# Kernel tuning notes

Measured on AMD Instinct MI355X. Metric: run time of the kernel, lower is better.

Reference implementation:

```python
import jax, jax.numpy as jnp
import numpy as np

N_NODES = 100000
N_EDGES = 3200000
IN_FEAT = 512
HIDDEN = 256
N_CLASS = 40


def setup_inputs() -> dict:
    key = jax.random.key(0)
    ks = jax.random.split(key, 6)
    x = jax.random.normal(ks[0], (N_NODES, IN_FEAT), dtype=jnp.float32)
    w1 = jax.random.uniform(ks[1], (IN_FEAT, HIDDEN), dtype=jnp.float32)
    b1 = jnp.zeros((HIDDEN,), dtype=jnp.float32)
    w2 = jax.random.uniform(ks[2], (HIDDEN, N_CLASS), dtype=jnp.float32)
    b2 = jnp.zeros((N_CLASS,), dtype=jnp.float32)
    edge_val = jax.random.uniform(ks[3], (N_EDGES,), dtype=jnp.float32)
    edge_row = jax.random.randint(ks[4], (N_EDGES,), 0, N_NODES, dtype=jnp.int32)
    edge_col = jax.random.randint(ks[5], (N_EDGES,), 0, N_NODES, dtype=jnp.int32)
    return {"x": x, "w1": w1, "b1": b1, "w2": w2, "b2": b2,
            "edge_val": edge_val, "edge_row": edge_row, "edge_col": edge_col}


def _graph_conv(h, w, b, edge_val, edge_row, edge_col, n_nodes):
    # dense transform: [N, d_in] @ [d_in, d_out]
    support = h @ w
    # sparse adj @ support via gather + segment_sum (COO SpMM)
    msgs = edge_val[:, None] * support[edge_col]          # [E, d_out]
    agg = jax.ops.segment_sum(msgs, edge_row, num_segments=n_nodes)
    return agg + b


def reference(x, w1, b1, w2, b2, edge_val, edge_row, edge_col):
    n = x.shape[0]
    h = jax.nn.relu(_graph_conv(x, w1, b1, edge_val, edge_row, edge_col, n))
    # dropout is identity in eval mode (training=False)
    out = _graph_conv(h, w2, b2, edge_val, edge_row, edge_col, n)
    return jax.nn.log_softmax(out, axis=1)
```

## Files before the change

kernel.cpp:

```cpp
#include <hip/hip_runtime.h>
#include <cstdint>
#include <cstddef>

#define N_NODES 100000
#define N_EDGES 3200000
#define IN_FEAT 512
#define HIDDEN  256
#define N_CLASS 40
#define S2_STRIDE 48

#define N_BUCKETS 196
#define SC_CHUNK 4096
#define N_SC_BLOCKS 782

#define OFF_SUPPORT1 ((size_t)0)
#define OFF_H        ((size_t)51200000)
#define OFF_SUPPORT2 ((size_t)102400000)
#define OFF_W1T      ((size_t)112000000)
#define OFF_W2T      ((size_t)112262144)
#define OFF_RPTR     ((size_t)112286976)
#define OFF_BCNT     ((size_t)112687104)
#define OFF_BBASE    ((size_t)112688128)
#define OFF_BCUR     ((size_t)112689152)
#define OFF_BINNED   ((size_t)112690176)
#define OFF_SEDGE    ((size_t)138290176)

typedef __attribute__((ext_vector_type(8))) short short8x;
typedef __attribute__((ext_vector_type(4))) float f32x4;
typedef __attribute__((ext_vector_type(8))) unsigned short u16x8;
typedef __attribute__((ext_vector_type(3))) unsigned int u32x3;
typedef __attribute__((ext_vector_type(4))) unsigned int u32x4;

static __device__ __forceinline__ unsigned short f2bf(float f) {
  unsigned u = __float_as_uint(f);
  unsigned r = (u + 0x7FFFu + ((u >> 16) & 1u)) >> 16;
  return (unsigned short)r;
}
static __device__ __forceinline__ float bf2f(unsigned short s) {
  return __uint_as_float(((unsigned)s) << 16);
}
static __device__ __forceinline__ float bflo(unsigned u) {
  return __uint_as_float(u << 16);
}
static __device__ __forceinline__ float bfhi(unsigned u) {
  return __uint_as_float(u & 0xFFFF0000u);
}

static __device__ __forceinline__ void gl16(const void* g, void* l) {
  __builtin_amdgcn_global_load_lds(
      (const __attribute__((address_space(1))) unsigned int*)g,
      (__attribute__((address_space(3))) unsigned int*)l, 16, 0, 0);
}

__global__ __launch_bounds__(256) void k_bincnt(const int* __restrict__ erow,
                                                int* __restrict__ bcnt,
                                                const float* __restrict__ W1,
                                                unsigned short* __restrict__ W1t,
                                                const float* __restrict__ W2,
                                                unsigned short* __restrict__ W2t) {
  int tid = blockIdx.x * 256 + threadIdx.x;
  {
    int n = tid & 255;
    int k = tid >> 8;
    W1t[(size_t)n * IN_FEAT + k] = f2bf(W1[(size_t)k * HIDDEN + n]);
  }
  if (tid < 48 * HIDDEN) {
    int n = tid >> 8;
    int k = tid & 255;
    W2t[n * HIDDEN + k] = (n < N_CLASS) ? f2bf(W2[(size_t)k * N_CLASS + n]) : 0;
  }
  __shared__ int lh[256];
  lh[threadIdx.x] = 0;
  __syncthreads();
  int i = tid;
  int stride = gridDim.x * blockDim.x;
  for (; i < N_EDGES; i += stride) atomicAdd(&lh[erow[i] >> 9], 1);
  __syncthreads();
  if (threadIdx.x < N_BUCKETS) atomicAdd(&bcnt[threadIdx.x], lh[threadIdx.x]);
}

__global__ __launch_bounds__(256) void k_binscan(const int* __restrict__ bcnt,
                                                 int* __restrict__ bbase,
                                                 int* __restrict__ bcur,
                                                 int* __restrict__ rptr) {
  __shared__ int s[256];
  int t = threadIdx.x;
  int v = (t < N_BUCKETS) ? bcnt[t] : 0;
  s[t] = v;
  __syncthreads();
  for (int off = 1; off < 256; off <<= 1) {
    int y = (t >= off) ? s[t - off] : 0;
    __syncthreads();
    s[t] += y;
    __syncthreads();
  }
  if (t < N_BUCKETS) {
    int e = s[t] - v;
    bbase[t] = e;
    bcur[t] = e;
  }
  if (t == 0) {
    bbase[N_BUCKETS] = N_EDGES;
    rptr[N_NODES] = N_EDGES;
  }
}

__global__ __launch_bounds__(256) void k_binscatter(const int* __restrict__ erow,
                                                    const int* __restrict__ ecol,
                                                    const float* __restrict__ eval,
                                                    int* __restrict__ bcur,
                                                    int2* __restrict__ binned) {
  __shared__ int lcnt[256];
  __shared__ int lcur[256];
  const int t = threadIdx.x;
  const int base = blockIdx.x * SC_CHUNK;
  lcnt[t] = 0;
  __syncthreads();
  int rows[16], cols[16], vals[16];
#pragma unroll
  for (int e = 0; e < 16; e++) {
    int i = base + t + e * 256;
    if (i < N_EDGES) {
      rows[e] = erow[i];
      cols[e] = ecol[i];
      vals[e] = __float_as_int(eval[i]);
      atomicAdd(&lcnt[rows[e] >> 9], 1);
    } else {
      rows[e] = -1;
    }
  }
  __syncthreads();
  if (t < N_BUCKETS) lcur[t] = atomicAdd(&bcur[t], lcnt[t]);
  __syncthreads();
#pragma unroll
  for (int e = 0; e < 16; e++) {
    if (rows[e] >= 0) {
      int bkt = rows[e] >> 9;
      int p = atomicAdd(&lcur[bkt], 1);
      binned[p] = make_int2(((rows[e] & 511) << 17) | cols[e], vals[e]);
    }
  }
}

__global__ __launch_bounds__(256) void k_bucket_csr(const int2* __restrict__ binned,
                                                    const int* __restrict__ bbase,
                                                    int* __restrict__ rptr,
                                                    int2* __restrict__ sedge) {
  const int b = blockIdx.x;
  const int t = threadIdx.x;
  __shared__ int cnt[512];
  __shared__ int excl[512];
  __shared__ int s[256];
  cnt[t] = 0;
  cnt[t + 256] = 0;
  __syncthreads();
  const int ebase = bbase[b];
  const int ecnt = bbase[b + 1] - ebase;
  for (int i = t; i < ecnt; i += 256)
    atomicAdd(&cnt[((unsigned)binned[ebase + i].x) >> 17], 1);
  __syncthreads();
  int c0 = cnt[2 * t], c1 = cnt[2 * t + 1];
  s[t] = c0 + c1;
  __syncthreads();
  for (int off = 1; off < 256; off <<= 1) {
    int y = (t >= off) ? s[t - off] : 0;
    __syncthreads();
    s[t] += y;
    __syncthreads();
  }
  int e = s[t] - (c0 + c1);
  excl[2 * t] = e;
  excl[2 * t + 1] = e + c0;
  __syncthreads();
  for (int i = t; i < 512; i += 256) {
    int node = b * 512 + i;
    if (node < N_NODES) rptr[node] = ebase + excl[i];
  }
  __syncthreads();
  for (int i = t; i < ecnt; i += 256) {
    int2 e2 = binned[ebase + i];
    int lrow = ((unsigned)e2.x) >> 17;
    int col = e2.x & 0x1FFFF;
    int p = atomicAdd(&excl[lrow], 1);
    sedge[ebase + p] = make_int2(col, e2.y);
  }
}

__global__ __launch_bounds__(256) void k_gemm1(const float* __restrict__ X,
                                               const unsigned short* __restrict__ Wt,
                                               unsigned short* __restrict__ C) {
  __shared__ float AsF[128 * 32];
  __shared__ unsigned short BsS[256 * 32];
  const int t = threadIdx.x;
  const int wave = t >> 6, lane = t & 63;
  const int q = lane >> 4, r = lane & 15;
  const int wm = (wave >> 1) * 64;
  const int wn = (wave & 1) * 128;
  const int m0 = blockIdx.x * 128;

  const int ar_base = wave * 8 + (lane >> 3);
  const int ac = lane & 7;
  const int br_base = wave * 16 + (lane >> 2);
  const int bc = lane & 3;

  f32x4 acc[4][8];
#pragma unroll
  for (int mi = 0; mi < 4; mi++)
#pragma unroll
    for (int ni = 0; ni < 8; ni++) acc[mi][ni] = (f32x4){0.f, 0.f, 0.f, 0.f};

  for (int k0 = 0; k0 < IN_FEAT; k0 += 32) {
#pragma unroll
    for (int j = 0; j < 4; j++) {
      int row = ar_base + j * 32;
      int gr = m0 + row;
      if (gr > N_NODES - 1) gr = N_NODES - 1;
      int gc = ac ^ (row & 7);
      gl16(&X[(size_t)gr * IN_FEAT + k0 + gc * 4],
           (char*)AsF + j * 4096 + wave * 1024);
    }
#pragma unroll
    for (int j = 0; j < 4; j++) {
      int row = br_base + j * 64;
      int gc = bc ^ (row & 3);
      gl16(&Wt[(size_t)row * IN_FEAT + k0 + gc * 8],
           (char*)BsS + j * 4096 + wave * 1024);
    }
    __syncthreads();

    short8x af[4];
#pragma unroll
    for (int mi = 0; mi < 4; mi++) {
      int row = wm + mi * 16 + r;
      int sw = row & 7;
      const float* Ar = &AsF[row * 32];
      f32x4 a0 = *(const f32x4*)&Ar[(((q << 1)) ^ sw) << 2];
      f32x4 a1 = *(const f32x4*)&Ar[(((q << 1) | 1) ^ sw) << 2];
      short8x a;
      a[0] = (short)f2bf(a0[0]); a[1] = (short)f2bf(a0[1]);
      a[2] = (short)f2bf(a0[2]); a[3] = (short)f2bf(a0[3]);
      a[4] = (short)f2bf(a1[0]); a[5] = (short)f2bf(a1[1]);
      a[6] = (short)f2bf(a1[2]); a[7] = (short)f2bf(a1[3]);
      af[mi] = a;
    }
#pragma unroll
    for (int ni = 0; ni < 8; ni++) {
      int row = wn + ni * 16 + r;
      short8x b = *(const short8x*)&BsS[row * 32 + ((q ^ (row & 3)) << 3)];
#pragma unroll
      for (int mi = 0; mi < 4; mi++)
        acc[mi][ni] = __builtin_amdgcn_mfma_f32_16x16x32_bf16(af[mi], b,
                                                              acc[mi][ni], 0, 0, 0);
    }
    __syncthreads();
  }
#pragma unroll
  for (int mi = 0; mi < 4; mi++) {
#pragma unroll
    for (int ni = 0; ni < 8; ni++) {
      int col = wn + ni * 16 + r;
#pragma unroll
      for (int reg = 0; reg < 4; reg++) {
        int row = m0 + wm + mi * 16 + q * 4 + reg;
        if (row < N_NODES)
          C[(size_t)row * HIDDEN + col] = f2bf(acc[mi][ni][reg]);
      }
    }
  }
}

__global__ __launch_bounds__(256) void k_spmm1(const unsigned short* __restrict__ S,
                                               const int* __restrict__ rptr,
                                               const int2* __restrict__ sedge,
                                               const float* __restrict__ b1,
                                               unsigned short* __restrict__ H,
                                               int node_off) {
  const int node = node_off + ((blockIdx.x * blockDim.x + threadIdx.x) >> 6);
  const int lane = threadIdx.x & 63;
  const int half = lane >> 5;
  const int fl = lane & 31;
  int e0 = rptr[node], e1 = rptr[node + 1];
  float a[8];
#pragma unroll
  for (int k = 0; k < 8; k++) a[k] = 0.f;
  for (int base = e0; base < e1; base += 64) {
    int rem = min(64, e1 - base);
    int c = 0;
    float v = 0.f;
    if (lane < rem) {
      int2 e = sedge[base + lane];
      c = e.x;
      v = __int_as_float(e.y);
    }
    int iters = (rem + 1) >> 1;
#pragma unroll 8
    for (int j = 0; j < iters; j++) {
      int idx = 2 * j + half;
      int cj = __shfl(c, idx);
      float vj = __shfl(v, idx);
      short8x s8 = *(const short8x*)&S[(size_t)cj * HIDDEN + fl * 8];
#pragma unroll
      for (int k = 0; k < 8; k++)
        a[k] += vj * bf2f((unsigned short)s8[k]);
    }
  }
#pragma unroll
  for (int k = 0; k < 8; k++) a[k] += __shfl_xor(a[k], 32);
  if (half == 0) {
    float4 b0 = *(const float4*)&b1[fl * 8];
    float4 b4 = *(const float4*)&b1[fl * 8 + 4];
    u16x8 o;
    o[0] = f2bf(fmaxf(a[0] + b0.x, 0.f));
    o[1] = f2bf(fmaxf(a[1] + b0.y, 0.f));
    o[2] = f2bf(fmaxf(a[2] + b0.z, 0.f));
    o[3] = f2bf(fmaxf(a[3] + b0.w, 0.f));
    o[4] = f2bf(fmaxf(a[4] + b4.x, 0.f));
    o[5] = f2bf(fmaxf(a[5] + b4.y, 0.f));
    o[6] = f2bf(fmaxf(a[6] + b4.z, 0.f));
    o[7] = f2bf(fmaxf(a[7] + b4.w, 0.f));
    *(u16x8*)&H[(size_t)node * HIDDEN + fl * 8] = o;
  }
}

__global__ __launch_bounds__(256) void k_gemm2(const unsigned short* __restrict__ H,
                                               const unsigned short* __restrict__ W2t,
                                               unsigned short* __restrict__ S2) {
  const int t = threadIdx.x;
  const int wave = t >> 6, lane = t & 63;
  const int q = lane >> 4, r = lane & 15;
  const int m0 = blockIdx.x * 64 + wave * 16;

  f32x4 acc[3];
#pragma unroll
  for (int n = 0; n < 3; n++) acc[n] = (f32x4){0.f, 0.f, 0.f, 0.f};

  int arow = m0 + r;
  if (arow > N_NODES - 1) arow = N_NODES - 1;
  const unsigned short* Arow = &H[(size_t)arow * HIDDEN + q * 8];

#pragma unroll
  for (int k0 = 0; k0 < HIDDEN; k0 += 32) {
    short8x af = *(const short8x*)&Arow[k0];
    short8x bf0 = *(const short8x*)&W2t[(0 * 16 + r) * HIDDEN + k0 + q * 8];
    short8x bf1 = *(const short8x*)&W2t[(1 * 16 + r) * HIDDEN + k0 + q * 8];
    short8x bf2 = *(const short8x*)&W2t[(2 * 16 + r) * HIDDEN + k0 + q * 8];
    acc[0] = __builtin_amdgcn_mfma_f32_16x16x32_bf16(af, bf0, acc[0], 0, 0, 0);
    acc[1] = __builtin_amdgcn_mfma_f32_16x16x32_bf16(af, bf1, acc[1], 0, 0, 0);
    acc[2] = __builtin_amdgcn_mfma_f32_16x16x32_bf16(af, bf2, acc[2], 0, 0, 0);
  }
#pragma unroll
  for (int n = 0; n < 3; n++) {
#pragma unroll
    for (int reg = 0; reg < 4; reg++) {
      int row = m0 + q * 4 + reg;
      if (row < N_NODES)
        S2[(size_t)row * S2_STRIDE + n * 16 + r] = f2bf(acc[n][reg]);
    }
  }
}

__global__ __launch_bounds__(256) void k_spmm2(const unsigned short* __restrict__ S2,
                                               const int* __restrict__ rptr,
                                               const int2* __restrict__ sedge,
                                               const float* __restrict__ b2,
                                               float* __restrict__ out) {
  const int node = (blockIdx.x * blockDim.x + threadIdx.x) >> 6;
  const int lane = threadIdx.x & 63;
  const int q = lane >> 3;
  const int fl = lane & 7;
  int e0 = rptr[node], e1 = rptr[node + 1];
  float a[6] = {0.f, 0.f, 0.f, 0.f, 0.f, 0.f};
  for (int base = e0; base < e1; base += 64) {
    int rem = min(64, e1 - base);
    int c = 0;
    float v = 0.f;
    if (lane < rem) {
      int2 e = sedge[base + lane];
      c = e.x;
      v = __int_as_float(e.y);
    }
    int iters = (rem + 7) >> 3;
#pragma unroll 8
    for (int j = 0; j < iters; j++) {
      int idx = 8 * j + q;
      int cj = __shfl(c, idx);
      float vj = __shfl(v, idx);
      u32x3 w = *(const u32x3*)&S2[(size_t)cj * S2_STRIDE + fl * 6];
      a[0] += vj * bflo(w.x);
      a[1] += vj * bfhi(w.x);
      a[2] += vj * bflo(w.y);
      a[3] += vj * bfhi(w.y);
      a[4] += vj * bflo(w.z);
      a[5] += vj * bfhi(w.z);
    }
  }
#pragma unroll
  for (int k = 0; k < 6; k++) {
    a[k] += __shfl_xor(a[k], 8);
    a[k] += __shfl_xor(a[k], 16);
    a[k] += __shfl_xor(a[k], 32);
  }
  float x[6];
  float mloc = -INFINITY;
#pragma unroll
  for (int k = 0; k < 6; k++) {
    int f = fl * 6 + k;
    x[k] = (f < N_CLASS) ? (a[k] + b2[f]) : -INFINITY;
    mloc = fmaxf(mloc, x[k]);
  }
#pragma unroll
  for (int o = 1; o < 8; o <<= 1) mloc = fmaxf(mloc, __shfl_xor(mloc, o));
  float sloc = 0.f;
#pragma unroll
  for (int k = 0; k < 6; k++)
    sloc += (fl * 6 + k < N_CLASS) ? expf(x[k] - mloc) : 0.f;
#pragma unroll
  for (int o = 1; o < 8; o <<= 1) sloc += __shfl_xor(sloc, o);
  float ls = logf(sloc);
  if (q == 0) {
#pragma unroll
    for (int k = 0; k < 6; k++) {
      int f = fl * 6 + k;
      if (f < N_CLASS) out[(size_t)node * N_CLASS + f] = (x[k] - mloc) - ls;
    }
  }
}

extern "C" void kernel_launch(void* const* d_in, const int* in_sizes, int n_in,
                              void* d_out, int out_size, void* d_ws, size_t ws_size,
                              hipStream_t stream) {
  const float* x    = (const float*)d_in[0];
  const float* w1   = (const float*)d_in[1];
  const float* b1   = (const float*)d_in[2];
  const float* w2   = (const float*)d_in[3];
  const float* b2   = (const float*)d_in[4];
  const float* eval = (const float*)d_in[5];
  const int*   erow = (const int*)d_in[6];
  const int*   ecol = (const int*)d_in[7];
  float* out = (float*)d_out;

  char* ws = (char*)d_ws;
  unsigned short* support1 = (unsigned short*)(ws + OFF_SUPPORT1);
  unsigned short* h        = (unsigned short*)(ws + OFF_H);
  unsigned short* support2 = (unsigned short*)(ws + OFF_SUPPORT2);
  unsigned short* w1t = (unsigned short*)(ws + OFF_W1T);
  unsigned short* w2t = (unsigned short*)(ws + OFF_W2T);
  int*   rptr   = (int*)(ws + OFF_RPTR);
  int*   bcnt   = (int*)(ws + OFF_BCNT);
  int*   bbase  = (int*)(ws + OFF_BBASE);
  int*   bcur   = (int*)(ws + OFF_BCUR);
  int2*  binned = (int2*)(ws + OFF_BINNED);
  int2*  sedge  = (int2*)(ws + OFF_SEDGE);

  hipMemsetAsync(bcnt, 0, N_BUCKETS * 4, stream);
  k_bincnt<<<512, 256, 0, stream>>>(erow, bcnt, w1, w1t, w2, w2t);
  k_binscan<<<1, 256, 0, stream>>>(bcnt, bbase, bcur, rptr);
  k_binscatter<<<N_SC_BLOCKS, 256, 0, stream>>>(erow, ecol, eval, bcur, binned);
  k_bucket_csr<<<N_BUCKETS, 256, 0, stream>>>(binned, bbase, rptr, sedge);

  k_gemm1<<<dim3((N_NODES + 127) / 128, 1), 256, 0, stream>>>(x, w1t, support1);
  k_spmm1<<<N_NODES / 8, 256, 0, stream>>>(support1, rptr, sedge, b1, h, 0);
  k_spmm1<<<N_NODES / 8, 256, 0, stream>>>(support1, rptr, sedge, b1, h, N_NODES / 2);

  k_gemm2<<<(N_NODES + 63) / 64, 256, 0, stream>>>(h, w2t, support2);
  k_spmm2<<<N_NODES / 4, 256, 0, stream>>>(support2, rptr, sedge, b2, out);
}
```

Baseline: 800.2 us.

## Double-buffer shared-memory tiles in the first GEMM to overlap loads with MFMA

The first GEMM kernel now keeps two shared-memory buffers for the X and W1 tiles. It prefetches the next K-slice with async global-to-LDS loads while computing on the current one, and drops the trailing barrier. Global pointers are precomputed once instead of per iteration. This aims to hide load latency behind the MFMA work, at the cost of doubling LDS use to 64KB, which may lower occupancy.

After: 797.7 us. No clear change (-0.3%).

```diff
diff --git a/kernel.cpp b/kernel.cpp
--- a/kernel.cpp
+++ b/kernel.cpp
@@ -189,8 +189,8 @@
 __global__ __launch_bounds__(256) void k_gemm1(const float* __restrict__ X,
                                                const unsigned short* __restrict__ Wt,
                                                unsigned short* __restrict__ C) {
-  __shared__ float AsF[128 * 32];
-  __shared__ unsigned short BsS[256 * 32];
+  __shared__ float AsF[2 * 128 * 32];
+  __shared__ unsigned short BsS[2 * 256 * 32];
   const int t = threadIdx.x;
   const int wave = t >> 6, lane = t & 63;
   const int q = lane >> 4, r = lane & 15;
@@ -203,37 +203,53 @@
   const int br_base = wave * 16 + (lane >> 2);
   const int bc = lane & 3;
 
+  const float* agp[4];
+  const unsigned short* bgp[4];
+#pragma unroll
+  for (int j = 0; j < 4; j++) {
+    int row = ar_base + j * 32;
+    int gr = m0 + row;
+    if (gr > N_NODES - 1) gr = N_NODES - 1;
+    agp[j] = &X[(size_t)gr * IN_FEAT + ((ac ^ (row & 7)) << 2)];
+    int brow = br_base + j * 64;
+    bgp[j] = &Wt[(size_t)brow * IN_FEAT + ((bc ^ (brow & 3)) << 3)];
+  }
+
   f32x4 acc[4][8];
 #pragma unroll
   for (int mi = 0; mi < 4; mi++)
 #pragma unroll
     for (int ni = 0; ni < 8; ni++) acc[mi][ni] = (f32x4){0.f, 0.f, 0.f, 0.f};
 
+#pragma unroll
+  for (int j = 0; j < 4; j++)
+    gl16(agp[j], (char*)AsF + j * 4096 + wave * 1024);
+#pragma unroll
+  for (int j = 0; j < 4; j++)
+    gl16(bgp[j], (char*)BsS + j * 4096 + wave * 1024);
+
+  int cur = 0;
   for (int k0 = 0; k0 < IN_FEAT; k0 += 32) {
-#pragma unroll
-    for (int j = 0; j < 4; j++) {
-      int row = ar_base + j * 32;
-      int gr = m0 + row;
-      if (gr > N_NODES - 1) gr = N_NODES - 1;
-      int gc = ac ^ (row & 7);
-      gl16(&X[(size_t)gr * IN_FEAT + k0 + gc * 4],
-           (char*)AsF + j * 4096 + wave * 1024);
-    }
-#pragma unroll
-    for (int j = 0; j < 4; j++) {
-      int row = br_base + j * 64;
-      int gc = bc ^ (row & 3);
-      gl16(&Wt[(size_t)row * IN_FEAT + k0 + gc * 8],
-           (char*)BsS + j * 4096 + wave * 1024);
-    }
     __syncthreads();
 
+    if (k0 + 32 < IN_FEAT) {
+      int nb = (cur ^ 1) * 16384;
+#pragma unroll
+      for (int j = 0; j < 4; j++)
+        gl16(agp[j] + k0 + 32, (char*)AsF + nb + j * 4096 + wave * 1024);
+#pragma unroll
+      for (int j = 0; j < 4; j++)
+        gl16(bgp[j] + k0 + 32, (char*)BsS + nb + j * 4096 + wave * 1024);
+    }
+
+    const float* Abuf = AsF + cur * 4096;
+    const unsigned short* Bbuf = BsS + cur * 8192;
     short8x af[4];
 #pragma unroll
     for (int mi = 0; mi < 4; mi++) {
       int row = wm + mi * 16 + r;
       int sw = row & 7;
-      const float* Ar = &AsF[row * 32];
+      const float* Ar = &Abuf[row * 32];
       f32x4 a0 = *(const f32x4*)&Ar[(((q << 1)) ^ sw) << 2];
       f32x4 a1 = *(const f32x4*)&Ar[(((q << 1) | 1) ^ sw) << 2];
       short8x a;
@@ -246,13 +262,13 @@
 #pragma unroll
     for (int ni = 0; ni < 8; ni++) {
       int row = wn + ni * 16 + r;
-      short8x b = *(const short8x*)&BsS[row * 32 + ((q ^ (row & 3)) << 3)];
+      short8x b = *(const short8x*)&Bbuf[row * 32 + ((q ^ (row & 3)) << 3)];
 #pragma unroll
       for (int mi = 0; mi < 4; mi++)
         acc[mi][ni] = __builtin_amdgcn_mfma_f32_16x16x32_bf16(af[mi], b,
                                                               acc[mi][ni], 0, 0, 0);
     }
-    __syncthreads();
+    cur ^= 1;
   }
 #pragma unroll
   for (int mi = 0; mi < 4; mi++) {
```
